# Kernel tuning notes

Hardware: AMD Instinct MI355X
Metric: run time of the kernel (lower is better)

## Reference

```python
import jax, jax.numpy as jnp
import numpy as np

NUM_OBJ = 32
OBJ_DIM = 128
MSG_W = 256
FIN_W = 256
BATCH = 256
BN_EPS = 1e-5
NEG_SLOPE = 0.01


def _linear_init(key, fan_in, fan_out):
    # torch nn.Linear default: U(-1/sqrt(fan_in), 1/sqrt(fan_in))
    kw, kb = jax.random.split(key)
    bound = 1.0 / np.sqrt(fan_in)
    w = jax.random.uniform(kw, (fan_out, fan_in), jnp.float32, -bound, bound)
    b = jax.random.uniform(kb, (fan_out,), jnp.float32, -bound, bound)
    return w, b


def setup_inputs() -> dict:
    key = jax.random.key(0)
    ks = jax.random.split(key, 8)
    state = jax.random.normal(ks[0], (BATCH, NUM_OBJ, OBJ_DIM), jnp.float32)
    edges = jax.random.randint(ks[1], (BATCH, NUM_OBJ * NUM_OBJ), 0, 2).astype(jnp.float32)
    msg_w1, msg_b1 = _linear_init(ks[2], OBJ_DIM * 2, MSG_W)
    msg_w2, msg_b2 = _linear_init(ks[3], MSG_W, OBJ_DIM)
    fin_w1, fin_b1 = _linear_init(ks[4], OBJ_DIM * 2, FIN_W)
    fin_w2, fin_b2 = _linear_init(ks[5], FIN_W, OBJ_DIM)
    msg_gamma = jnp.ones((MSG_W,), jnp.float32)
    msg_beta = jnp.zeros((MSG_W,), jnp.float32)
    fin_gamma = jnp.ones((FIN_W,), jnp.float32)
    fin_beta = jnp.zeros((FIN_W,), jnp.float32)
    return {
        "state": state, "edges": edges,
        "msg_w1": msg_w1, "msg_b1": msg_b1, "msg_gamma": msg_gamma, "msg_beta": msg_beta,
        "msg_w2": msg_w2, "msg_b2": msg_b2,
        "fin_w1": fin_w1, "fin_b1": fin_b1, "fin_gamma": fin_gamma, "fin_beta": fin_beta,
        "fin_w2": fin_w2, "fin_b2": fin_b2,
    }


def _batchnorm_train(x, gamma, beta):
    # training-mode BatchNorm1d: batch stats over rows, biased variance
    mean = jnp.mean(x, axis=0)
    var = jnp.mean(jnp.square(x - mean), axis=0)
    return (x - mean) * jax.lax.rsqrt(var + BN_EPS) * gamma + beta


def _mlp(x, w1, b1, gamma, beta, w2, b2):
    h = x @ w1.T + b1
    h = _batchnorm_train(h, gamma, beta)
    h = jnp.where(h >= 0, h, NEG_SLOPE * h)  # LeakyReLU
    return h @ w2.T + b2


def reference(state, edges, msg_w1, msg_b1, msg_gamma, msg_beta, msg_w2, msg_b2,
              fin_w1, fin_b1, fin_gamma, fin_beta, fin_w2, fin_b2):
    B, n, d = state.shape
    src = jnp.repeat(jnp.arange(n), n)   # [n*n]
    tgt = jnp.tile(jnp.arange(n), n)     # [n*n]
    sources = state[:, src]              # [B, n*n, d]
    targets = state[:, tgt]              # [B, n*n, d]
    e = edges[:, :, None]                # [B, n*n, 1]
    need = jnp.concatenate([sources * e, targets * e], axis=2)  # [B, n*n, 2d]
    msgs = _mlp(need.reshape(-1, 2 * d), msg_w1, msg_b1, msg_gamma, msg_beta, msg_w2, msg_b2)
    agg = jnp.sum(msgs.reshape(B, n, n, d), axis=2)  # sum over inner edge group
    sm = jnp.concatenate([state, agg], axis=2).reshape(-1, 2 * d)
    out = _mlp(sm, fin_w1, fin_b1, fin_gamma, fin_beta, fin_w2, fin_b2)
    return out.reshape(B, n, d)
```

## Files before the change

### kernel.cpp

```cpp
#include <hip/hip_runtime.h>

#define NPAIR  262144
#define BN_EPS 1e-5f

typedef unsigned short u16;
typedef unsigned int   u32;
typedef __attribute__((ext_vector_type(8))) short bf16x8;
typedef __attribute__((ext_vector_type(4))) float f32x4;
typedef __attribute__((ext_vector_type(4))) unsigned short u16x4;
typedef __attribute__((ext_vector_type(4))) unsigned int u32x4;

__device__ __forceinline__ u16 f2bf(float f) {
    union { float f; unsigned u; } v; v.f = f;
    unsigned r = v.u + 0x7fffu + ((v.u >> 16) & 1u);
    return (u16)(r >> 16);
}
__device__ __forceinline__ float bf2f(u16 u) {
    union { unsigned u; float f; } v; v.u = ((unsigned)u) << 16; return v.f;
}
__device__ __forceinline__ u16x4 cvt4(float4 v) {
    u16x4 r;
    r[0] = f2bf(v.x); r[1] = f2bf(v.y); r[2] = f2bf(v.z); r[3] = f2bf(v.w);
    return r;
}
__device__ __forceinline__ bf16x8 cvt8_f32(const float* p) {
    f32x4 v0 = *(const f32x4*)p, v1 = *(const f32x4*)(p + 4);
    bf16x8 r;
    #pragma unroll
    for (int k = 0; k < 4; ++k) {
        r[k]     = (short)f2bf(v0[k]);
        r[4 + k] = (short)f2bf(v1[k]);
    }
    return r;
}
__device__ __forceinline__ bf16x8 cvt8_bn_b(const u16* p, const float* a, const float* d) {
    u16x4 v0 = *(const u16x4*)p, v1 = *(const u16x4*)(p + 4);
    f32x4 a0 = *(const f32x4*)a, a1 = *(const f32x4*)(a + 4);
    f32x4 d0 = *(const f32x4*)d, d1 = *(const f32x4*)(d + 4);
    bf16x8 r;
    #pragma unroll
    for (int k = 0; k < 4; ++k) {
        float x0 = fmaf(a0[k], bf2f(v0[k]), d0[k]); x0 = fmaxf(x0, 0.01f * x0);
        float x1 = fmaf(a1[k], bf2f(v1[k]), d1[k]); x1 = fmaxf(x1, 0.01f * x1);
        r[k]     = (short)f2bf(x0);
        r[4 + k] = (short)f2bf(x1);
    }
    return r;
}

__global__ __launch_bounds__(256) void prep_kernel(
    const float* __restrict__ w1, const float4* __restrict__ w2,
    const float4* __restrict__ fw1, const float4* __restrict__ fw2,
    u16x4* __restrict__ W1b, u16x4* __restrict__ W2b,
    u16x4* __restrict__ FW1b, u16x4* __restrict__ FW2b,
    f32x4* __restrict__ sums)
{
    int g = blockIdx.x * 256 + threadIdx.x;
    if (g < 16384) {
        const int o = g * 4, n = o >> 7, k = o & 127;
        const float4 v = *(const float4*)(w1 + (n < 256 ? n * 256 + k
                                                        : (n - 256) * 256 + 128 + k));
        W1b[g] = cvt4(v); return;
    }
    g -= 16384;
    if (g < 8192) { W2b[g] = cvt4(w2[g]); return; }
    g -= 8192;
    if (g < 16384) { FW1b[g] = cvt4(fw1[g]); return; }
    g -= 16384;
    if (g < 8192) { FW2b[g] = cvt4(fw2[g]); return; }
    g -= 8192;
    if (g < 264) { const f32x4 z = {}; sums[g] = z; }
}

__global__ __launch_bounds__(1024) void pq_stats(
    const float* __restrict__ state, const u16* __restrict__ W1b,
    const float* __restrict__ edges, const float* __restrict__ b1,
    u16* __restrict__ PQb, float* __restrict__ sums)
{
    __shared__ float Qls[33 * 256];
    __shared__ float redA[16 * 256];
    __shared__ float redB[16 * 256];
    __shared__ u32 masks[32];
    __shared__ __align__(16) unsigned char list8[32 * 32];
    __shared__ float cdf[32];

    const int b    = blockIdx.x;
    const int t    = threadIdx.x;
    const int lane = t & 63;
    const int w    = t >> 6;
    const int lr   = lane & 15;
    const int lk   = (lane >> 4) * 8;
    const int c0   = lane * 4;

    if (t < 256) ((u32*)list8)[t] = 0x20202020u;
    if (t < 64) { const f32x4 z = {}; *(f32x4*)&Qls[32 * 256 + t * 4] = z; }

    const float ev = edges[(size_t)b * 1024 + t];

    const int col0 = w * 32;
    f32x4 acc[2][2] = {};
    #pragma unroll
    for (int ks = 0; ks < 4; ++ks) {
        const int kabs = ks * 32 + lk;
        bf16x8 af[2];
        #pragma unroll
        for (int rf = 0; rf < 2; ++rf)
            af[rf] = cvt8_f32(state + (size_t)(b * 32 + rf * 16 + lr) * 128 + kabs);
        #pragma unroll
        for (int cf = 0; cf < 2; ++cf) {
            const bf16x8 bfr = *(const bf16x8*)(W1b + (size_t)(col0 + cf * 16 + lr) * 128 + kabs);
            #pragma unroll
            for (int rf = 0; rf < 2; ++rf)
                acc[rf][cf] = __builtin_amdgcn_mfma_f32_16x16x32_bf16(af[rf], bfr, acc[rf][cf], 0, 0, 0);
        }
    }
    #pragma unroll
    for (int rf = 0; rf < 2; ++rf)
        #pragma unroll
        for (int cf = 0; cf < 2; ++cf) {
            const int col = col0 + cf * 16 + lr;
            #pragma unroll
            for (int r = 0; r < 4; ++r) {
                const int row = rf * 16 + (lane >> 4) * 4 + r;
                const u16 u = f2bf(acc[rf][cf][r]);
                PQb[(size_t)(b * 32 + row) * 512 + col] = u;
                if (col >= 256) Qls[row * 256 + (col - 256)] = bf2f(u);
            }
        }
    __syncthreads();

    {
        const int il_t = t >> 5;
        const int j_t  = t & 31;
        const unsigned long long bal = __ballot(ev != 0.f);
        const u32 m32 = (lane < 32) ? (u32)bal : (u32)(bal >> 32);
        if (ev != 0.f)
            list8[il_t * 32 + __popc(m32 & ((1u << j_t) - 1u))] = (unsigned char)j_t;
        if (j_t == 0) masks[il_t] = m32;
    }
    __syncthreads();

    if (t < 32) {
        u32 cnt = 0;
        #pragma unroll
        for (int i = 0; i < 32; ++i) cnt += (masks[i] >> t) & 1u;
        cdf[t] = (float)cnt;
    }
    if (t == 0) {
        int tot = 0;
        #pragma unroll
        for (int i = 0; i < 32; ++i) tot += __popc(masks[i]);
        atomicAdd(&sums[512], (float)tot);
    }

    const f32x4 b14 = *(const f32x4*)(b1 + c0);
    f32x4 sumA = {}, sumB = {};

    #pragma unroll
    for (int ii = 0; ii < 2; ++ii) {
        const int il = 2 * w + ii;
        const int n1 = __popc(masks[il]);
        const int npad = (n1 + 3) & ~3;
        const float frd = (float)n1;
        f32x4 eq = {};
        const u32x4 l0 = *(const u32x4*)(list8 + il * 32);
        const u32x4 l1 = *(const u32x4*)(list8 + il * 32 + 16);
        const u32 wbuf[8] = {l0[0], l0[1], l0[2], l0[3], l1[0], l1[1], l1[2], l1[3]};
        #pragma unroll
        for (int wi = 0; wi < 8; ++wi) {
            if (wi * 4 >= npad) break;
            const u32 w4 = wbuf[wi];
            #pragma unroll
            for (int kb = 0; kb < 4; ++kb) {
                const int j = (w4 >> (kb * 8)) & 0xff;
                const f32x4 q = *(const f32x4*)&Qls[j * 256 + c0];
                #pragma unroll
                for (int k = 0; k < 4; ++k) eq[k] += q[k];
            }
        }
        const u16x4 pu = *(const u16x4*)(PQb + (size_t)(b * 32 + il) * 512 + c0);
        #pragma unroll
        for (int k = 0; k < 4; ++k) {
            const float pb = bf2f(pu[k]) + b14[k];
            sumA[k] += frd * pb + eq[k];
            sumB[k] = fmaf(frd * pb + 2.f * eq[k], pb, sumB[k]);
        }
    }
    __syncthreads();

    #pragma unroll
    for (int jj = 0; jj < 2; ++jj) {
        const int j = 2 * w + jj;
        const float cdj = cdf[j];
        const f32x4 q = *(const f32x4*)&Qls[j * 256 + c0];
        #pragma unroll
        for (int k = 0; k < 4; ++k) sumB[k] = fmaf(cdj * q[k], q[k], sumB[k]);
    }
    *(f32x4*)&redA[w * 256 + c0] = sumA;
    *(f32x4*)&redB[w * 256 + c0] = sumB;
    __syncthreads();
    if (t < 256) {
        float a = 0.f, bb = 0.f;
        #pragma unroll
        for (int ww = 0; ww < 16; ++ww) {
            a  += redA[ww * 256 + t];
            bb += redB[ww * 256 + t];
        }
        atomicAdd(&sums[t], a);
        atomicAdd(&sums[256 + t], bb);
    }
}

__global__ __launch_bounds__(512) void s_agg_h2_kernel(
    const u16* __restrict__ PQb, const float* __restrict__ edges,
    const float* __restrict__ sums, const float* __restrict__ gamma,
    const float* __restrict__ beta, const float* __restrict__ b1,
    const float* __restrict__ state,
    const u16* __restrict__ W2b, const float* __restrict__ b2,
    const u16* __restrict__ FW1b, const float* __restrict__ fb1,
    u16* __restrict__ H2b, float* __restrict__ sums2)
{
    __shared__ float Qls[33 * 256];
    __shared__ u16 Ssb[16 * 256];
    __shared__ u16 Asb[16 * 128];
    __shared__ u16 aggs[16 * 128];
    __shared__ __align__(16) unsigned char list8[16 * 32];
    __shared__ int n1s[16];
    __shared__ float sred[512];

    const int b    = blockIdx.x;
    const int i0   = blockIdx.y * 16;
    const int t    = threadIdx.x;
    const int lane = t & 63;
    const int w    = t >> 6;
    const int lr   = lane & 15;
    const int lkg  = lane >> 4;
    const int lk   = lkg * 8;
    const int c0   = lane * 4;

    sred[t] = 0.f;

    const float Etot = sums[512];
    const float nz   = (float)NPAIR - Etot;
    const float invN = 1.f / (float)NPAIR;
    const f32x4 s1  = *(const f32x4*)(sums + c0);
    const f32x4 s2  = *(const f32x4*)(sums + 256 + c0);
    const f32x4 g4  = *(const f32x4*)(gamma + c0);
    const f32x4 be4 = *(const f32x4*)(beta + c0);
    const f32x4 b14 = *(const f32x4*)(b1 + c0);
    f32x4 a4, d4, ld4;
    #pragma unroll
    for (int k = 0; k < 4; ++k) {
        const float mean = (s1[k] + nz * b14[k]) * invN;
        const float ms   = (s2[k] + nz * b14[k] * b14[k]) * invN;
        const float var  = fmaf(-mean, mean, ms);
        a4[k]  = g4[k] * rsqrtf(var + BN_EPS);
        d4[k]  = fmaf(b14[k] - mean, a4[k], be4[k]);
        ld4[k] = fmaxf(d4[k], 0.01f * d4[k]);
    }

    #pragma unroll
    for (int it = 0; it < 4; ++it) {
        const int row = w + it * 8;
        const u16x4 qu = *(const u16x4*)(PQb + (size_t)(b * 32 + row) * 512 + 256 + c0);
        f32x4 q;
        #pragma unroll
        for (int k = 0; k < 4; ++k) q[k] = a4[k] * bf2f(qu[k]);
        *(f32x4*)&Qls[row * 256 + c0] = q;
    }
    if (t < 256) {
        const int row = t >> 4, k8 = (t & 15) * 8;
        const bf16x8 av = cvt8_f32(state + (size_t)(b * 32 + i0 + row) * 128 + k8);
        *(bf16x8*)((char*)Asb + ((row * 256 + k8 * 2) ^ ((row & 7) << 4))) = av;
    }
    if (t < 64) { const f32x4 z = {}; *(f32x4*)&Qls[32 * 256 + t * 4] = z; }
    if (t < 128) ((u32*)list8)[t] = 0x20202020u;

    const float ev = edges[(size_t)b * 1024 + (i0 + (t >> 5)) * 32 + (t & 31)];
    __syncthreads();

    {
        const int il_t = t >> 5;
        const int j_t  = t & 31;
        const unsigned long long bal = __ballot(ev != 0.f);
        const u32 m32 = (lane < 32) ? (u32)bal : (u32)(bal >> 32);
        if (ev != 0.f)
            list8[il_t * 32 + __popc(m32 & ((1u << j_t) - 1u))] = (unsigned char)j_t;
        if (j_t == 0) n1s[il_t] = __popc(m32);
    }
    __syncthreads();

    #pragma unroll
    for (int ii = 0; ii < 2; ++ii) {
        const int il = 2 * w + ii;
        const int gi = b * 32 + i0 + il;
        const int n1 = n1s[il];
        const int npad = (n1 + 3) & ~3;
        const float frd = (float)n1;
        const float fz = (float)(32 - n1);
        const float fp = (float)(npad - n1);
        const u16x4 pu = *(const u16x4*)(PQb + (size_t)gi * 512 + c0);
        f32x4 ap, absacc, linq = {};
        #pragma unroll
        for (int k = 0; k < 4; ++k) {
            ap[k] = fmaf(a4[k], bf2f(pu[k]), d4[k]);
            absacc[k] = -fp * fabsf(ap[k]);
        }
        const u32x4 l0 = *(const u32x4*)(list8 + il * 32);
        const u32x4 l1 = *(const u32x4*)(list8 + il * 32 + 16);
        const u32 wbuf[8] = {l0[0], l0[1], l0[2], l0[3], l1[0], l1[1], l1[2], l1[3]};
        #pragma unroll
        for (int wi = 0; wi < 8; ++wi) {
            if (wi * 4 >= npad) break;
            const u32 w4 = wbuf[wi];
            #pragma unroll
            for (int kb = 0; kb < 4; ++kb) {
                const int j = (w4 >> (kb * 8)) & 0xff;
                const f32x4 q = *(const f32x4*)&Qls[j * 256 + c0];
                #pragma unroll
                for (int k = 0; k < 4; ++k) {
                    absacc[k] += fabsf(ap[k] + q[k]);
                    linq[k]   += q[k];
                }
            }
        }
        u16x4 o;
        #pragma unroll
        for (int k = 0; k < 4; ++k) {
            const float lin = fmaf(frd, ap[k], linq[k]);
            const float S = fmaf(fz, ld4[k], fmaf(0.505f, lin, 0.495f * absacc[k]));
            o[k] = f2bf(S);
        }
        *(u16x4*)((char*)Ssb + il * 512 + ((lane * 8) ^ ((il & 7) << 4))) = o;
    }
    __syncthreads();

    {
        f32x4 acc2 = {};
        #pragma unroll
        for (int ks = 0; ks < 8; ++ks) {
            const int rdoff = (ks * 64 + lkg * 16) ^ ((lr & 7) << 4);
            const bf16x8 afr = *(const bf16x8*)((const char*)Ssb + lr * 512 + rdoff);
            const bf16x8 bfr = *(const bf16x8*)(W2b + (size_t)(w * 16 + lr) * 256 + ks * 32 + lk);
            acc2 = __builtin_amdgcn_mfma_f32_16x16x32_bf16(afr, bfr, acc2, 0, 0, 0);
        }
        const int col = w * 16 + lr;
        const float bv = 32.f * b2[col];
        #pragma unroll
        for (int r = 0; r < 4; ++r) {
            const int row = lkg * 4 + r;
            *(u16*)((char*)aggs + ((row * 256 + col * 2) ^ ((row & 7) << 4))) = f2bf(acc2[r] + bv);
        }
    }
    __syncthreads();

    {
        f32x4 acc3[2] = {};
        #pragma unroll
        for (int ks = 0; ks < 8; ++ks) {
            const int kabs = ks * 32 + lk;
            const int row = lr;
            bf16x8 af3;
            if (ks < 4)
                af3 = *(const bf16x8*)((const char*)Asb + ((row * 256 + kabs * 2) ^ ((row & 7) << 4)));
            else
                af3 = *(const bf16x8*)((const char*)aggs + ((row * 256 + (kabs - 128) * 2) ^ ((row & 7) << 4)));
            #pragma unroll
            for (int cf = 0; cf < 2; ++cf) {
                const int col = w * 32 + cf * 16 + lr;
                const bf16x8 bfr = *(const bf16x8*)(FW1b + (size_t)col * 256 + kabs);
                acc3[cf] = __builtin_amdgcn_mfma_f32_16x16x32_bf16(af3, bfr, acc3[cf], 0, 0, 0);
            }
        }
        #pragma unroll
        for (int cf = 0; cf < 2; ++cf) {
            const int col = w * 32 + cf * 16 + lr;
            const float bv = fb1[col];
            float s = 0.f, ss = 0.f;
            #pragma unroll
            for (int r = 0; r < 4; ++r) {
                const int row = lkg * 4 + r;
                const float v = acc3[cf][r] + bv;
                H2b[(size_t)(b * 32 + i0 + row) * 256 + col] = f2bf(v);
                s += v;
                ss = fmaf(v, v, ss);
            }
            atomicAdd(&sred[col], s);
            atomicAdd(&sred[256 + col], ss);
        }
    }
    __syncthreads();
    if (t < 256) {
        atomicAdd(&sums2[t], sred[t]);
        atomicAdd(&sums2[256 + t], sred[256 + t]);
    }
}

__global__ __launch_bounds__(256) void out_gemm(
    const u16* __restrict__ H2b, const u16* __restrict__ FW2b,
    const float* __restrict__ fb2, const float* __restrict__ sums2,
    const float* __restrict__ gamma, const float* __restrict__ beta,
    float* __restrict__ out)
{
    __shared__ float adl[512];
    const int t = threadIdx.x;
    {
        const float invR = 1.f / 8192.f;
        const float mean = sums2[t] * invR;
        const float var  = fmaf(-mean, mean, sums2[256 + t] * invR);
        const float a    = gamma[t] * rsqrtf(var + BN_EPS);
        adl[t]       = a;
        adl[256 + t] = fmaf(-mean, a, beta[t]);
    }
    __syncthreads();

    const int lane = t & 63;
    const int wave = t >> 6;
    const int row0 = blockIdx.y * 64 + wave * 16;
    const int col0 = blockIdx.x * 32;
    const int lr = lane & 15;
    const int lk = (lane >> 4) * 8;

    f32x4 acc[2] = {};
    #pragma unroll
    for (int ks = 0; ks < 8; ++ks) {
        const int kabs = ks * 32 + lk;
        const bf16x8 af = cvt8_bn_b(H2b + (size_t)(row0 + lr) * 256 + kabs,
                                    adl + kabs, adl + 256 + kabs);
        #pragma unroll
        for (int cf = 0; cf < 2; ++cf) {
            const bf16x8 bf = *(const bf16x8*)(FW2b + (size_t)(col0 + cf * 16 + lr) * 256 + kabs);
            acc[cf] = __builtin_amdgcn_mfma_f32_16x16x32_bf16(af, bf, acc[cf], 0, 0, 0);
        }
    }
    #pragma unroll
    for (int cf = 0; cf < 2; ++cf) {
        const int col = col0 + cf * 16 + lr;
        const float bv = fb2[col];
        #pragma unroll
        for (int r = 0; r < 4; ++r) {
            const int row = row0 + (lane >> 4) * 4 + r;
            out[(size_t)row * 128 + col] = acc[cf][r] + bv;
        }
    }
}

extern "C" void kernel_launch(void* const* d_in, const int* in_sizes, int n_in,
                              void* d_out, int out_size, void* d_ws, size_t ws_size,
                              hipStream_t stream)
{
    const float* state     = (const float*)d_in[0];
    const float* edges     = (const float*)d_in[1];
    const float* msg_w1    = (const float*)d_in[2];
    const float* msg_b1    = (const float*)d_in[3];
    const float* msg_gamma = (const float*)d_in[4];
    const float* msg_beta  = (const float*)d_in[5];
    const float* msg_w2    = (const float*)d_in[6];
    const float* msg_b2    = (const float*)d_in[7];
    const float* fin_w1    = (const float*)d_in[8];
    const float* fin_b1    = (const float*)d_in[9];
    const float* fin_gamma = (const float*)d_in[10];
    const float* fin_beta  = (const float*)d_in[11];
    const float* fin_w2    = (const float*)d_in[12];
    const float* fin_b2    = (const float*)d_in[13];

    char* w = (char*)d_ws;
    u16*   PQb  = (u16*)(w);
    u16*   H2b  = (u16*)(w + 8388608);
    u16*   W1b  = (u16*)(w + 12582912);
    u16*   W2b  = (u16*)(w + 12713984);
    u16*   FW1b = (u16*)(w + 12779520);
    u16*   FW2b = (u16*)(w + 12910592);
    float* sums = (float*)(w + 12976128);
    float* sums2 = sums + 544;

    prep_kernel<<<194, 256, 0, stream>>>(
        msg_w1, (const float4*)msg_w2, (const float4*)fin_w1, (const float4*)fin_w2,
        (u16x4*)W1b, (u16x4*)W2b, (u16x4*)FW1b, (u16x4*)FW2b, (f32x4*)sums);

    pq_stats<<<256, 1024, 0, stream>>>(state, W1b, edges, msg_b1, PQb, sums);

    s_agg_h2_kernel<<<dim3(256, 2), 512, 0, stream>>>(
        PQb, edges, sums, msg_gamma, msg_beta, msg_b1,
        state, W2b, msg_b2, FW1b, fin_b1, H2b, sums2);

    out_gemm<<<dim3(4, 128), 256, 0, stream>>>(
        H2b, FW2b, fin_b2, sums2, fin_gamma, fin_beta, (float*)d_out);
}
```

Before: 67.00 us.

## Fuse output GEMM into aggregation kernel via software grid barrier

Merges the final BN+LeakyReLU+GEMM into the s_agg_h2 kernel. H2 is kept in swizzled shared memory instead of a global buffer, and a software grid-wide barrier waits for the global BN statistics before the output GEMM runs. This drops one kernel launch and the H2 round trip through global memory. In exchange, every block must be co-resident (512 blocks, launch_bounds min 4 blocks per CU), and the spin barrier can deadlock if occupancy or LDS limits prevent that.

```diff
diff --git a/kernel.cpp b/kernel.cpp
--- a/kernel.cpp
+++ b/kernel.cpp
@@ -2,6 +2,7 @@
 
 #define NPAIR  262144
 #define BN_EPS 1e-5f
+#define NBLK2  512
 
 typedef unsigned short u16;
 typedef unsigned int   u32;
@@ -33,7 +34,7 @@
     }
     return r;
 }
-__device__ __forceinline__ bf16x8 cvt8_bn_b(const u16* p, const float* a, const float* d) {
+__device__ __forceinline__ bf16x8 cvt8_bn_lds(const u16* p, const float* a, const float* d) {
     u16x4 v0 = *(const u16x4*)p, v1 = *(const u16x4*)(p + 4);
     f32x4 a0 = *(const f32x4*)a, a1 = *(const f32x4*)(a + 4);
     f32x4 d0 = *(const f32x4*)d, d1 = *(const f32x4*)(d + 4);
@@ -48,12 +49,28 @@
     return r;
 }
 
+__device__ __forceinline__ void gridbar(u32* cnt, u32* gen) {
+    __syncthreads();
+    __threadfence();
+    if (threadIdx.x == 0) {
+        const u32 g = __hip_atomic_load(gen, __ATOMIC_ACQUIRE, __HIP_MEMORY_SCOPE_AGENT);
+        const u32 old = __hip_atomic_fetch_add(cnt, 1, __ATOMIC_ACQ_REL, __HIP_MEMORY_SCOPE_AGENT);
+        if (old == NBLK2 - 1) {
+            __hip_atomic_store(cnt, 0, __ATOMIC_RELEASE, __HIP_MEMORY_SCOPE_AGENT);
+            __hip_atomic_fetch_add(gen, 1, __ATOMIC_ACQ_REL, __HIP_MEMORY_SCOPE_AGENT);
+        } else {
+            while (__hip_atomic_load(gen, __ATOMIC_ACQUIRE, __HIP_MEMORY_SCOPE_AGENT) == g) {}
+        }
+    }
+    __syncthreads();
+}
+
 __global__ __launch_bounds__(256) void prep_kernel(
     const float* __restrict__ w1, const float4* __restrict__ w2,
     const float4* __restrict__ fw1, const float4* __restrict__ fw2,
     u16x4* __restrict__ W1b, u16x4* __restrict__ W2b,
     u16x4* __restrict__ FW1b, u16x4* __restrict__ FW2b,
-    f32x4* __restrict__ sums)
+    f32x4* __restrict__ sums4, u32* __restrict__ bar)
 {
     int g = blockIdx.x * 256 + threadIdx.x;
     if (g < 16384) {
@@ -69,7 +86,8 @@
     g -= 16384;
     if (g < 8192) { FW2b[g] = cvt4(fw2[g]); return; }
     g -= 8192;
-    if (g < 264) { const f32x4 z = {}; sums[g] = z; }
+    if (g < 264) { const f32x4 z = {}; sums4[g] = z; return; }
+    if (g == 264) { bar[0] = 0; bar[1] = 0; }
 }
 
 __global__ __launch_bounds__(1024) void pq_stats(
@@ -211,22 +229,27 @@
     }
 }
 
-__global__ __launch_bounds__(512) void s_agg_h2_kernel(
+__global__ __launch_bounds__(512, 4) void s_agg_h2_out_kernel(
     const u16* __restrict__ PQb, const float* __restrict__ edges,
     const float* __restrict__ sums, const float* __restrict__ gamma,
     const float* __restrict__ beta, const float* __restrict__ b1,
     const float* __restrict__ state,
     const u16* __restrict__ W2b, const float* __restrict__ b2,
     const u16* __restrict__ FW1b, const float* __restrict__ fb1,
-    u16* __restrict__ H2b, float* __restrict__ sums2)
+    const u16* __restrict__ FW2b, const float* __restrict__ fb2,
+    const float* __restrict__ g2, const float* __restrict__ be2,
+    float* __restrict__ sums2, u32* __restrict__ bar,
+    float* __restrict__ out)
 {
     __shared__ float Qls[33 * 256];
     __shared__ u16 Ssb[16 * 256];
     __shared__ u16 Asb[16 * 128];
     __shared__ u16 aggs[16 * 128];
+    __shared__ u16 H2s[16 * 256];
     __shared__ __align__(16) unsigned char list8[16 * 32];
     __shared__ int n1s[16];
     __shared__ float sred[512];
+    __shared__ float adl[512];
 
     const int b    = blockIdx.x;
     const int i0   = blockIdx.y * 16;
@@ -381,7 +404,7 @@
             for (int r = 0; r < 4; ++r) {
                 const int row = lkg * 4 + r;
                 const float v = acc3[cf][r] + bv;
-                H2b[(size_t)(b * 32 + i0 + row) * 256 + col] = f2bf(v);
+                *(u16*)((char*)H2s + ((row * 512 + col * 2) ^ ((row & 7) << 4))) = f2bf(v);
                 s += v;
                 ss = fmaf(v, v, ss);
             }
@@ -394,53 +417,35 @@
         atomicAdd(&sums2[t], sred[t]);
         atomicAdd(&sums2[256 + t], sred[256 + t]);
     }
-}
-
-__global__ __launch_bounds__(256) void out_gemm(
-    const u16* __restrict__ H2b, const u16* __restrict__ FW2b,
-    const float* __restrict__ fb2, const float* __restrict__ sums2,
-    const float* __restrict__ gamma, const float* __restrict__ beta,
-    float* __restrict__ out)
-{
-    __shared__ float adl[512];
-    const int t = threadIdx.x;
-    {
+
+    gridbar(&bar[0], &bar[1]);
+
+    if (t < 256) {
         const float invR = 1.f / 8192.f;
         const float mean = sums2[t] * invR;
         const float var  = fmaf(-mean, mean, sums2[256 + t] * invR);
-        const float a    = gamma[t] * rsqrtf(var + BN_EPS);
+        const float a    = g2[t] * rsqrtf(var + BN_EPS);
         adl[t]       = a;
-        adl[256 + t] = fmaf(-mean, a, beta[t]);
-    }
-    __syncthreads();
-
-    const int lane = t & 63;
-    const int wave = t >> 6;
-    const int row0 = blockIdx.y * 64 + wave * 16;
-    const int col0 = blockIdx.x * 32;
-    const int lr = lane & 15;
-    const int lk = (lane >> 4) * 8;
-
-    f32x4 acc[2] = {};
-    #pragma unroll
-    for (int ks = 0; ks < 8; ++ks) {
-        const int kabs = ks * 32 + lk;
-        const bf16x8 af = cvt8_bn_b(H2b + (size_t)(row0 + lr) * 256 + kabs,
-                                    adl + kabs, adl + 256 + kabs);
-        #pragma unroll
-        for (int cf = 0; cf < 2; ++cf) {
-            const bf16x8 bf = *(const bf16x8*)(FW2b + (size_t)(col0 + cf * 16 + lr) * 256 + kabs);
-            acc[cf] = __builtin_amdgcn_mfma_f32_16x16x32_bf16(af, bf, acc[cf], 0, 0, 0);
-        }
-    }
-    #pragma unroll
-    for (int cf = 0; cf < 2; ++cf) {
-        const int col = col0 + cf * 16 + lr;
+        adl[256 + t] = fmaf(-mean, a, be2[t]);
+    }
+    __syncthreads();
+
+    {
+        f32x4 acc4 = {};
+        #pragma unroll
+        for (int ks = 0; ks < 8; ++ks) {
+            const int kabs = ks * 32 + lk;
+            const u16* hp = (const u16*)((const char*)H2s + ((lr * 512 + kabs * 2) ^ ((lr & 7) << 4)));
+            const bf16x8 af4 = cvt8_bn_lds(hp, adl + kabs, adl + 256 + kabs);
+            const bf16x8 bfr = *(const bf16x8*)(FW2b + (size_t)(w * 16 + lr) * 256 + kabs);
+            acc4 = __builtin_amdgcn_mfma_f32_16x16x32_bf16(af4, bfr, acc4, 0, 0, 0);
+        }
+        const int col = w * 16 + lr;
         const float bv = fb2[col];
         #pragma unroll
         for (int r = 0; r < 4; ++r) {
-            const int row = row0 + (lane >> 4) * 4 + r;
-            out[(size_t)row * 128 + col] = acc[cf][r] + bv;
+            const int row = lkg * 4 + r;
+            out[(size_t)(b * 32 + i0 + row) * 128 + col] = acc4[r] + bv;
         }
     }
 }
@@ -466,24 +471,22 @@
 
     char* w = (char*)d_ws;
     u16*   PQb  = (u16*)(w);
-    u16*   H2b  = (u16*)(w + 8388608);
-    u16*   W1b  = (u16*)(w + 12582912);
-    u16*   W2b  = (u16*)(w + 12713984);
-    u16*   FW1b = (u16*)(w + 12779520);
-    u16*   FW2b = (u16*)(w + 12910592);
-    float* sums = (float*)(w + 12976128);
+    u16*   W1b  = (u16*)(w + 8388608);
+    u16*   W2b  = (u16*)(w + 8519680);
+    u16*   FW1b = (u16*)(w + 8585216);
+    u16*   FW2b = (u16*)(w + 8716288);
+    float* sums = (float*)(w + 8781824);
     float* sums2 = sums + 544;
+    u32*   bar  = (u32*)(w + 8786176);
 
     prep_kernel<<<194, 256, 0, stream>>>(
         msg_w1, (const float4*)msg_w2, (const float4*)fin_w1, (const float4*)fin_w2,
-        (u16x4*)W1b, (u16x4*)W2b, (u16x4*)FW1b, (u16x4*)FW2b, (f32x4*)sums);
+        (u16x4*)W1b, (u16x4*)W2b, (u16x4*)FW1b, (u16x4*)FW2b, (f32x4*)sums, bar);
 
     pq_stats<<<256, 1024, 0, stream>>>(state, W1b, edges, msg_b1, PQb, sums);
 
-    s_agg_h2_kernel<<<dim3(256, 2), 512, 0, stream>>>(
+    s_agg_h2_out_kernel<<<dim3(256, 2), 512, 0, stream>>>(
         PQb, edges, sums, msg_gamma, msg_beta, msg_b1,
-        state, W2b, msg_b2, FW1b, fin_b1, H2b, sums2);
-
-    out_gemm<<<dim3(4, 128), 256, 0, stream>>>(
-        H2b, FW2b, fin_b2, sums2, fin_gamma, fin_beta, (float*)d_out);
-}
+        state, W2b, msg_b2, FW1b, fin_b1, FW2b, fin_b2,
+        fin_gamma, fin_beta, sums2, bar, (float*)d_out);
+}
```

After: 179.0 us. 167% more time.
